# Optimization experiments

Hardware: AMD Instinct MI355X
Metric: run time of the kernel (lower is better)

The kernel has to match this reference:

```python
import jax, jax.numpy as jnp
import numpy as np

HEAD_DIM = 64

def setup_inputs() -> dict:
    key = jax.random.key(0)
    k1, k2, k3, k4 = jax.random.split(key, 4)
    B, T, C, D = 8, 2048, 1024, HEAD_DIM
    x = jax.random.normal(k1, (B, T, C), dtype=jnp.float32)
    Wq = jax.random.normal(k2, (C, D), dtype=jnp.float32) * (1.0 / np.sqrt(C))
    Wk = jax.random.normal(k3, (C, D), dtype=jnp.float32) * (1.0 / np.sqrt(C))
    Wv = jax.random.normal(k4, (C, D), dtype=jnp.float32) * (1.0 / np.sqrt(C))
    return {"x": x, "Wq": Wq, "Wk": Wk, "Wv": Wv}

def reference(x, Wq, Wk, Wv):
    B, T, C = x.shape
    D = Wq.shape[1]
    q = jnp.einsum('btc,cd->btd', x, Wq)
    k = jnp.einsum('btc,cd->btd', x, Wk)
    v = jnp.einsum('btc,cd->btd', x, Wv)
    scale = 1.0 / jnp.sqrt(jnp.asarray(D, dtype=x.dtype))
    wei = jnp.einsum('bqd,bkd->bqk', q, k) * scale  # [B,T,T]
    causal = jnp.tril(jnp.ones((T, T), dtype=bool))
    wei = jnp.where(causal[None, :, :], wei, -jnp.inf)
    wei = jax.nn.softmax(wei, axis=-1)
    # dropout p=0.0 (eval) -> identity
    out = jnp.einsum('bqk,bkd->bqd', wei, v)  # [B,T,D]
    return out
```

## Files before the change

kernel.cpp:

```cpp
#include <hip/hip_runtime.h>
#include <hip/hip_bf16.h>


typedef __attribute__((ext_vector_type(8))) short short8;
typedef __attribute__((ext_vector_type(4))) float f32x4;

#define MFMA16(a, b, c) __builtin_amdgcn_mfma_f32_16x16x32_bf16((a), (b), (c), 0, 0, 0)

__device__ __forceinline__ unsigned short f2bf(float f) {
  unsigned int u = __builtin_bit_cast(unsigned int, f);
  unsigned int r = 0x7fffu + ((u >> 16) & 1u);
  return (unsigned short)((u + r) >> 16);
}

#define BATCH 8
#define SEQ   2048
#define CDIM  1024
#define DDIM  64
#define NTOK  (BATCH * SEQ)
#define LOG2E 1.44269504f

__global__ __launch_bounds__(256) void wt_kernel(const float* __restrict__ Wq,
                                                 const float* __restrict__ Wk,
                                                 const float* __restrict__ Wv,
                                                 unsigned short* __restrict__ WT) {
  int tid = blockIdx.x * 256 + threadIdx.x;
  int c    = tid & 63;
  int rest = tid >> 6;
  int k    = rest & 1023;
  int wi   = rest >> 10;
  const float* W = (wi == 0) ? Wq : ((wi == 1) ? Wk : Wv);
  float v = W[k * DDIM + c];
  if (wi == 0) v *= 0.125f * LOG2E;
  int row  = wi * 64 + c;
  int step = k >> 6;
  int col  = k & 63;
  size_t idx = (size_t)step * 12288 + (size_t)row * 64 +
               (size_t)(((col >> 3) ^ (row & 7)) * 8) + (col & 7);
  WT[idx] = f2bf(v);
}

__global__ __launch_bounds__(512) void proj_kernel(const float* __restrict__ x,
                                                   const unsigned short* __restrict__ WT,
                                                   unsigned short* __restrict__ qws,
                                                   unsigned short* __restrict__ kws,
                                                   unsigned short* __restrict__ vtws) {
  __shared__ __align__(16) unsigned short xs[2][32 * 64];
  __shared__ __align__(16) unsigned short wl[2][192 * 64];

  const int tid  = threadIdx.x;
  const int lane = tid & 63;
  const int w    = tid >> 6;
  const int wm   = w & 1;
  const int wn   = w >> 1;
  const int c16  = lane & 15;
  const int hi   = lane >> 4;
  const int n0   = blockIdx.x * 32;
  const bool xldr = (tid < 256);
  const int trow = (tid >> 3) & 31;
  const int kch  = tid & 7;

  f32x4 acc[3];
#pragma unroll
  for (int ct = 0; ct < 3; ++ct) acc[ct] = (f32x4){0.f, 0.f, 0.f, 0.f};

  const float* xbase = x + (size_t)(n0 + trow) * CDIM + kch * 8;
  const int xsw = trow * 64 + ((kch ^ (trow & 7)) * 8);

  const unsigned short* wsrc = WT + (size_t)w * 1536 + (size_t)lane * 8;
  auto stage_wt = [&](int step, int bufi) {
    const unsigned short* s = wsrc + (size_t)step * 12288;
    unsigned short* d = &wl[bufi][w * 1536];
#pragma unroll
    for (int j = 0; j < 3; ++j)
      __builtin_amdgcn_global_load_lds(
          (const __attribute__((address_space(1))) void*)(s + j * 512),
          (__attribute__((address_space(3))) void*)(d + j * 512), 16, 0, 0);
  };
  auto xstore = [&](f32x4 a, f32x4 b, int bufi) {
    short8 h;
#pragma unroll
    for (int j = 0; j < 4; ++j) { h[j] = (short)f2bf(a[j]); h[4 + j] = (short)f2bf(b[j]); }
    *reinterpret_cast<short8*>(&xs[bufi][xsw]) = h;
  };

  f32x4 xa1 = {0,0,0,0}, xb1 = xa1, xa2 = xa1, xb2 = xa1;
  if (xldr) {
    f32x4 a0 = *reinterpret_cast<const f32x4*>(xbase);
    f32x4 b0 = *reinterpret_cast<const f32x4*>(xbase + 4);
    xstore(a0, b0, 0);
    xa1 = *reinterpret_cast<const f32x4*>(xbase + 64);
    xb1 = *reinterpret_cast<const f32x4*>(xbase + 64 + 4);
  }
  stage_wt(0, 0);
  __syncthreads();

  int cur = 0;
  for (int st = 0; st < 16; ++st) {
    if (st + 2 < 16 && xldr) {
      xa2 = *reinterpret_cast<const f32x4*>(xbase + (st + 2) * 64);
      xb2 = *reinterpret_cast<const f32x4*>(xbase + (st + 2) * 64 + 4);
    }
    if (st + 1 < 16) stage_wt(st + 1, cur ^ 1);

    short8 bfrag[2];
    {
      int r = wm * 16 + c16;
#pragma unroll
      for (int f = 0; f < 2; ++f)
        bfrag[f] = *reinterpret_cast<const short8*>(
            &xs[cur][r * 64 + (((f * 4 + hi) ^ (r & 7)) * 8)]);
    }
#pragma unroll
    for (int ct = 0; ct < 3; ++ct) {
      int ra = (wn * 3 + ct) * 16 + c16;
#pragma unroll
      for (int f = 0; f < 2; ++f) {
        short8 af = *reinterpret_cast<const short8*>(
            &wl[cur][ra * 64 + (((f * 4 + hi) ^ (ra & 7)) * 8)]);
        acc[ct] = MFMA16(af, bfrag[f], acc[ct]);
      }
    }

    if (st + 1 < 16 && xldr) xstore(xa1, xb1, cur ^ 1);
    __syncthreads();
    xa1 = xa2; xb1 = xb2;
    cur ^= 1;
  }

  {
    const int token = n0 + wm * 16 + c16;
    const int b = token >> 11;
    const int t = token & 2047;
#pragma unroll
    for (int ct = 0; ct < 3; ++ct) {
      int cg = (wn * 3 + ct) * 16 + hi * 4;
      unsigned short h[4];
#pragma unroll
      for (int r = 0; r < 4; ++r) h[r] = f2bf(acc[ct][r]);
      if (cg < 64) {
        *reinterpret_cast<ushort4*>(qws + (size_t)token * DDIM + cg) =
            make_ushort4(h[0], h[1], h[2], h[3]);
      } else if (cg < 128) {
        *reinterpret_cast<ushort4*>(kws + (size_t)token * DDIM + (cg - 64)) =
            make_ushort4(h[0], h[1], h[2], h[3]);
      } else {
        int cv = cg - 128;
#pragma unroll
        for (int r = 0; r < 4; ++r)
          vtws[(size_t)(b * DDIM + cv + r) * SEQ + t] = h[r];
      }
    }
  }
}

__global__ __launch_bounds__(256) void attn_partial(const unsigned short* __restrict__ qws,
                                                    const unsigned short* __restrict__ kws,
                                                    const unsigned short* __restrict__ vtws,
                                                    float* __restrict__ po,
                                                    float* __restrict__ pml,
                                                    int MAXCH, int CHUNK) {
  __shared__ __align__(16) unsigned short kt[2][64 * 64];
  __shared__ __align__(16) unsigned short vt[2][64 * 64];
  __shared__ unsigned short pt[4][64 * 26];

  const int qt = blockIdx.x;
  const int ch = blockIdx.y;
  const int b  = blockIdx.z;

  const int kv_end = qt * 64 + 64;
  const int kv0_ch = ch * CHUNK;
  if (kv0_ch >= kv_end) return;
  const int block_lim = min(kv0_ch + CHUNK, kv_end);
  const int nt = (block_lim - kv0_ch + 63) >> 6;

  const int tid  = threadIdx.x;
  const int lane = tid & 63;
  const int w    = tid >> 6;
  const int c    = lane & 15;
  const int hi   = lane >> 4;
  const int qr0  = qt * 64 + w * 16;
  const int q    = qr0 + c;
  const int kv_last = qr0 + 15;

  const unsigned short* qb = qws + (size_t)b * SEQ * DDIM;
  short8 aq0 = *reinterpret_cast<const short8*>(qb + (size_t)q * DDIM + hi * 8);
  short8 aq1 = *reinterpret_cast<const short8*>(qb + (size_t)q * DDIM + 32 + hi * 8);

  float m = -INFINITY, l = 0.f;
  f32x4 o[4];
#pragma unroll
  for (int dn = 0; dn < 4; ++dn) o[dn] = (f32x4){0.f, 0.f, 0.f, 0.f};

  unsigned short* pw = pt[w];
  const unsigned short* kb = kws + (size_t)b * SEQ * DDIM;
  const unsigned short* vb = vtws + (size_t)b * DDIM * SEQ;

  auto stage_kv = [&](int bufi, int kv0) {
#pragma unroll
    for (int j = 0; j < 2; ++j) {
      int p   = w * 128 + j * 64 + lane;
      int row = p >> 3;
      int chk = (p & 7) ^ (row & 7);
      __builtin_amdgcn_global_load_lds(
          (const __attribute__((address_space(1))) void*)(kb + (size_t)(kv0 + row) * DDIM + chk * 8),
          (__attribute__((address_space(3))) void*)(&kt[bufi][w * 1024 + j * 512]), 16, 0, 0);
      __builtin_amdgcn_global_load_lds(
          (const __attribute__((address_space(1))) void*)(vb + (size_t)row * SEQ + kv0 + chk * 8),
          (__attribute__((address_space(3))) void*)(&vt[bufi][w * 1024 + j * 512]), 16, 0, 0);
    }
  };

  stage_kv(0, kv0_ch);
  __syncthreads();

  int cur = 0;
  for (int t = 0; t < nt; ++t) {
    const int kv0 = kv0_ch + t * 64;
    if (t + 1 < nt) stage_kv(cur ^ 1, kv0 + 64);

    if (kv0 <= kv_last) {
      f32x4 s[4];
#pragma unroll
      for (int n = 0; n < 4; ++n) {
        if (kv0 + n * 16 > kv_last) {
          s[n] = (f32x4){-INFINITY, -INFINITY, -INFINITY, -INFINITY};
          continue;
        }
        const unsigned short* kr = &kt[cur][(n * 16 + c) * 64];
        short8 ka0 = *reinterpret_cast<const short8*>(kr + ((hi ^ (c & 7)) * 8));
        short8 ka1 = *reinterpret_cast<const short8*>(kr + (((4 + hi) ^ (c & 7)) * 8));
        f32x4 z = (f32x4){0.f, 0.f, 0.f, 0.f};
        z = MFMA16(ka0, aq0, z);
        s[n] = MFMA16(ka1, aq1, z);
      }

      if (kv0 + 63 > qr0) {
#pragma unroll
        for (int n = 0; n < 4; ++n)
#pragma unroll
          for (int r = 0; r < 4; ++r)
            if (kv0 + n * 16 + hi * 4 + r > q) s[n][r] = -INFINITY;
      }

      float mx = -INFINITY;
#pragma unroll
      for (int n = 0; n < 4; ++n)
        mx = fmaxf(mx, fmaxf(fmaxf(s[n][0], s[n][1]), fmaxf(s[n][2], s[n][3])));
      mx = fmaxf(mx, __shfl_xor(mx, 16, 64));
      mx = fmaxf(mx, __shfl_xor(mx, 32, 64));

      float nm = fmaxf(m, mx);
      float sc = __builtin_exp2f(m - nm);
      m = nm;

      float ssum = 0.f;
#pragma unroll
      for (int n = 0; n < 4; ++n)
#pragma unroll
        for (int r = 0; r < 4; ++r) {
          float pv = __builtin_exp2f(s[n][r] - nm);
          pw[(n * 16 + hi * 4 + r) * 26 + c] = f2bf(pv);
          ssum += pv;
        }
      ssum += __shfl_xor(ssum, 16, 64);
      ssum += __shfl_xor(ssum, 32, 64);
      l = l * sc + ssum;

#pragma unroll
      for (int dn = 0; dn < 4; ++dn) o[dn] *= sc;

      const int nf = (kv0 + 32 <= kv_last) ? 2 : 1;
      for (int f = 0; f < nf; ++f) {
        short8 bp;
#pragma unroll
        for (int j = 0; j < 8; ++j)
          bp[j] = (short)pw[(f * 32 + hi * 8 + j) * 26 + c];
#pragma unroll
        for (int dn = 0; dn < 4; ++dn) {
          const unsigned short* vr = &vt[cur][(dn * 16 + c) * 64];
          short8 va = *reinterpret_cast<const short8*>(vr + (((f * 4 + hi) ^ (c & 7)) * 8));
          o[dn] = MFMA16(va, bp, o[dn]);
        }
      }
    }

    __syncthreads();
    cur ^= 1;
  }

  float* pob = po + (((size_t)(b * 32 + qt) * MAXCH + ch) * 64 + w * 16 + c) * 64 + hi * 4;
#pragma unroll
  for (int dn = 0; dn < 4; ++dn)
    *reinterpret_cast<f32x4*>(pob + dn * 16) = o[dn];

  if (hi == 0) {
    *reinterpret_cast<float2*>(
        pml + (((size_t)(b * 32 + qt) * MAXCH + ch) * 64 + w * 16 + c) * 2) =
        make_float2(m, l);
  }
}

__global__ __launch_bounds__(256) void attn_combine(const float* __restrict__ po,
                                                    const float* __restrict__ pml,
                                                    float* __restrict__ out,
                                                    int MAXCH, int CHUNK) {
  const int qt = blockIdx.x;
  const int b  = blockIdx.y;
  const int tid = threadIdx.x;
  const int row = tid >> 2;
  const int cg  = tid & 3;
  const int nch = (qt * 64 + 64 + CHUNK - 1) / CHUNK;

  const size_t base = (size_t)(b * 32 + qt) * MAXCH;

  float M = -INFINITY;
  for (int ch = 0; ch < nch; ++ch)
    M = fmaxf(M, pml[(base + ch) * 128 + row * 2]);

  float L = 0.f;
  f32x4 a0 = {0.f,0.f,0.f,0.f}, a1 = a0, a2 = a0, a3 = a0;
  for (int ch = 0; ch < nch; ++ch) {
    float mv = pml[(base + ch) * 128 + row * 2];
    float lv = pml[(base + ch) * 128 + row * 2 + 1];
    float wgt = __builtin_exp2f(mv - M);
    L += wgt * lv;
    const float* p = po + (base + ch) * 4096 + row * 64 + cg * 16;
    a0 += wgt * *reinterpret_cast<const f32x4*>(p);
    a1 += wgt * *reinterpret_cast<const f32x4*>(p + 4);
    a2 += wgt * *reinterpret_cast<const f32x4*>(p + 8);
    a3 += wgt * *reinterpret_cast<const f32x4*>(p + 12);
  }
  float invL = 1.f / L;
  float* ob = out + ((size_t)b * SEQ + qt * 64 + row) * 64 + cg * 16;
  *reinterpret_cast<f32x4*>(ob)      = a0 * invL;
  *reinterpret_cast<f32x4*>(ob + 4)  = a1 * invL;
  *reinterpret_cast<f32x4*>(ob + 8)  = a2 * invL;
  *reinterpret_cast<f32x4*>(ob + 12) = a3 * invL;
}

extern "C" void kernel_launch(void* const* d_in, const int* in_sizes, int n_in,
                              void* d_out, int out_size, void* d_ws, size_t ws_size,
                              hipStream_t stream) {
  const float* x  = (const float*)d_in[0];
  const float* Wq = (const float*)d_in[1];
  const float* Wk = (const float*)d_in[2];
  const float* Wv = (const float*)d_in[3];
  float* out = (float*)d_out;

  unsigned short* qws  = (unsigned short*)d_ws;
  unsigned short* kws  = qws + (size_t)NTOK * DDIM;
  unsigned short* vtws = kws + (size_t)NTOK * DDIM;
  unsigned short* WT   = vtws + (size_t)NTOK * DDIM;
  size_t fixed_end = (size_t)NTOK * DDIM * 3 * 2 + 192 * 1024 * 2;

  int MAXCH = 1;
  {
    const int cand[4] = {8, 4, 2, 1};
    for (int i = 0; i < 4; ++i) {
      size_t need = fixed_end +
                    (size_t)cand[i] * (8ull * 32 * 64 * 64 * 4 + 8ull * 32 * 64 * 2 * 4);
      if (need <= ws_size) { MAXCH = cand[i]; break; }
    }
  }

  wt_kernel<<<768, 256, 0, stream>>>(Wq, Wk, Wv, WT);
  proj_kernel<<<NTOK / 32, 512, 0, stream>>>(x, WT, qws, kws, vtws);

  float* po  = (float*)((char*)d_ws + fixed_end);
  float* pml = po + (size_t)BATCH * 32 * MAXCH * 64 * 64;
  int CHUNK = SEQ / MAXCH;
  attn_partial<<<dim3(32, MAXCH, BATCH), 256, 0, stream>>>(qws, kws, vtws, po, pml,
                                                           MAXCH, CHUNK);
  attn_combine<<<dim3(32, BATCH), 256, 0, stream>>>(po, pml, out, MAXCH, CHUNK);
}
```

Measured before the change: 65.80 us.

## Vectorize P tile LDS layout, lighten barriers, cap split-KV chunks at four

The per-wave P tile moves from a padded strided layout with scalar 16-bit stores and gathers to a fragment-ordered layout. Each lane now writes four bf16 values at once and reads its MFMA operand with a single 16-byte load. The __syncthreads calls become an explicit vmcnt wait plus s_barrier, and the final barrier is skipped on the last iteration. Split-KV chunk count is capped at 4 instead of 8, and the combine kernel is unrolled to four fixed chunk slots. Fewer chunks means longer serial KV loops per block but less partial-output traffic and combine work.

```diff
diff --git a/kernel.cpp b/kernel.cpp
--- a/kernel.cpp
+++ b/kernel.cpp
@@ -162,7 +162,7 @@
                                                     int MAXCH, int CHUNK) {
   __shared__ __align__(16) unsigned short kt[2][64 * 64];
   __shared__ __align__(16) unsigned short vt[2][64 * 64];
-  __shared__ unsigned short pt[4][64 * 26];
+  __shared__ __align__(16) unsigned short pt[4][1024];
 
   const int qt = blockIdx.x;
   const int ch = blockIdx.y;
@@ -192,7 +192,7 @@
 #pragma unroll
   for (int dn = 0; dn < 4; ++dn) o[dn] = (f32x4){0.f, 0.f, 0.f, 0.f};
 
-  unsigned short* pw = pt[w];
+  unsigned short* pwv = pt[w];
   const unsigned short* kb = kws + (size_t)b * SEQ * DDIM;
   const unsigned short* vb = vtws + (size_t)b * DDIM * SEQ;
 
@@ -212,7 +212,8 @@
   };
 
   stage_kv(0, kv0_ch);
-  __syncthreads();
+  asm volatile("s_waitcnt vmcnt(0)" ::: "memory");
+  __builtin_amdgcn_s_barrier();
 
   int cur = 0;
   for (int t = 0; t < nt; ++t) {
@@ -256,13 +257,16 @@
 
       float ssum = 0.f;
 #pragma unroll
-      for (int n = 0; n < 4; ++n)
-#pragma unroll
-        for (int r = 0; r < 4; ++r) {
-          float pv = __builtin_exp2f(s[n][r] - nm);
-          pw[(n * 16 + hi * 4 + r) * 26 + c] = f2bf(pv);
-          ssum += pv;
-        }
+      for (int n = 0; n < 4; ++n) {
+        float pv0 = __builtin_exp2f(s[n][0] - nm);
+        float pv1 = __builtin_exp2f(s[n][1] - nm);
+        float pv2 = __builtin_exp2f(s[n][2] - nm);
+        float pv3 = __builtin_exp2f(s[n][3] - nm);
+        ssum += (pv0 + pv1) + (pv2 + pv3);
+        ushort4 h4 = make_ushort4(f2bf(pv0), f2bf(pv1), f2bf(pv2), f2bf(pv3));
+        *reinterpret_cast<ushort4*>(
+            pwv + (2 * n + (hi >> 1)) * 128 + c * 8 + (hi & 1) * 4) = h4;
+      }
       ssum += __shfl_xor(ssum, 16, 64);
       ssum += __shfl_xor(ssum, 32, 64);
       l = l * sc + ssum;
@@ -272,10 +276,7 @@
 
       const int nf = (kv0 + 32 <= kv_last) ? 2 : 1;
       for (int f = 0; f < nf; ++f) {
-        short8 bp;
-#pragma unroll
-        for (int j = 0; j < 8; ++j)
-          bp[j] = (short)pw[(f * 32 + hi * 8 + j) * 26 + c];
+        short8 bp = *reinterpret_cast<const short8*>(pwv + (f * 4 + hi) * 128 + c * 8);
 #pragma unroll
         for (int dn = 0; dn < 4; ++dn) {
           const unsigned short* vr = &vt[cur][(dn * 16 + c) * 64];
@@ -285,7 +286,10 @@
       }
     }
 
-    __syncthreads();
+    if (t + 1 < nt) {
+      asm volatile("s_waitcnt vmcnt(0)" ::: "memory");
+      __builtin_amdgcn_s_barrier();
+    }
     cur ^= 1;
   }
 
@@ -310,27 +314,33 @@
   const int tid = threadIdx.x;
   const int row = tid >> 2;
   const int cg  = tid & 3;
-  const int nch = (qt * 64 + 64 + CHUNK - 1) / CHUNK;
+  const int nch = min((qt * 64 + 64 + CHUNK - 1) / CHUNK, MAXCH);
 
   const size_t base = (size_t)(b * 32 + qt) * MAXCH;
 
-  float M = -INFINITY;
-  for (int ch = 0; ch < nch; ++ch)
-    M = fmaxf(M, pml[(base + ch) * 128 + row * 2]);
+  float mv0 = -INFINITY, mv1 = -INFINITY, mv2 = -INFINITY, mv3 = -INFINITY;
+  float lv0 = 0, lv1 = 0, lv2 = 0, lv3 = 0;
+#define LOADML(i) if (i < nch) { \
+    float2 t = *reinterpret_cast<const float2*>(pml + (base + i) * 128 + row * 2); \
+    mv##i = t.x; lv##i = t.y; }
+  LOADML(0) LOADML(1) LOADML(2) LOADML(3)
+#undef LOADML
+
+  float M = fmaxf(fmaxf(mv0, mv1), fmaxf(mv2, mv3));
 
   float L = 0.f;
   f32x4 a0 = {0.f,0.f,0.f,0.f}, a1 = a0, a2 = a0, a3 = a0;
-  for (int ch = 0; ch < nch; ++ch) {
-    float mv = pml[(base + ch) * 128 + row * 2];
-    float lv = pml[(base + ch) * 128 + row * 2 + 1];
-    float wgt = __builtin_exp2f(mv - M);
-    L += wgt * lv;
-    const float* p = po + (base + ch) * 4096 + row * 64 + cg * 16;
-    a0 += wgt * *reinterpret_cast<const f32x4*>(p);
-    a1 += wgt * *reinterpret_cast<const f32x4*>(p + 4);
-    a2 += wgt * *reinterpret_cast<const f32x4*>(p + 8);
-    a3 += wgt * *reinterpret_cast<const f32x4*>(p + 12);
-  }
+#define ACC(i) if (i < nch) { \
+    float wgt = __builtin_exp2f(mv##i - M); \
+    L += wgt * lv##i; \
+    const float* p = po + (base + i) * 4096 + row * 64 + cg * 16; \
+    a0 += wgt * *reinterpret_cast<const f32x4*>(p); \
+    a1 += wgt * *reinterpret_cast<const f32x4*>(p + 4); \
+    a2 += wgt * *reinterpret_cast<const f32x4*>(p + 8); \
+    a3 += wgt * *reinterpret_cast<const f32x4*>(p + 12); }
+  ACC(0) ACC(1) ACC(2) ACC(3)
+#undef ACC
+
   float invL = 1.f / L;
   float* ob = out + ((size_t)b * SEQ + qt * 64 + row) * 64 + cg * 16;
   *reinterpret_cast<f32x4*>(ob)      = a0 * invL;
@@ -356,8 +366,8 @@
 
   int MAXCH = 1;
   {
-    const int cand[4] = {8, 4, 2, 1};
-    for (int i = 0; i < 4; ++i) {
+    const int cand[3] = {4, 2, 1};
+    for (int i = 0; i < 3; ++i) {
       size_t need = fixed_end +
                     (size_t)cand[i] * (8ull * 32 * 64 * 64 * 4 + 8ull * 32 * 64 * 2 * 4);
       if (need <= ws_size) { MAXCH = cand[i]; break; }
```

New measurement: 60.40 us. -8.2%, faster.
